# Optimization experiments

Hardware: AMD Instinct MI355X
Metric: run time of the kernel (lower is better)

## Reference

```python
import jax, jax.numpy as jnp
import numpy as np

B, T, C = 2, 2048, 2048
N_HEADS, HEAD_DIM = 16, 128
THETA = 10000.0


def _rope_cos_sin(T, dim, theta=THETA):
    inv_freq = 1.0 / (theta ** (jnp.arange(0, dim, 2, dtype=jnp.float32) / dim))  # (dim/2,)
    t = jnp.arange(T, dtype=jnp.float32)
    freqs = jnp.outer(t, inv_freq)  # (T, dim/2)
    return jnp.cos(freqs), jnp.sin(freqs)


def _apply_rope(x, cos, sin):
    # x: (B, H, T, D); cos/sin: (T, D/2) -> broadcast over B, H
    xr = x[..., 0::2]
    xi = x[..., 1::2]
    or_ = xr * cos - xi * sin
    oi_ = xr * sin + xi * cos
    return jnp.stack([or_, oi_], axis=-1).reshape(x.shape)


def setup_inputs() -> dict:
    key = jax.random.key(0)
    ks = jax.random.split(key, 5)
    scale = 1.0 / np.sqrt(C)
    x = jax.random.normal(ks[0], (B, T, C), dtype=jnp.float32)
    wq = jax.random.normal(ks[1], (C, N_HEADS * HEAD_DIM), dtype=jnp.float32) * scale
    wk = jax.random.normal(ks[2], (C, N_HEADS * HEAD_DIM), dtype=jnp.float32) * scale
    wv = jax.random.normal(ks[3], (C, N_HEADS * HEAD_DIM), dtype=jnp.float32) * scale
    wo = jax.random.normal(ks[4], (N_HEADS * HEAD_DIM, C), dtype=jnp.float32) * scale
    mask = jnp.tril(jnp.ones((T, T), dtype=bool))[None, None]  # causal (1,1,T,T)
    return {"x": x, "mask": mask, "wq": wq, "wk": wk, "wv": wv, "wo": wo}


def reference(x, mask, wq, wk, wv, wo):
    Bx, Tx, Cx = x.shape
    cos, sin = _rope_cos_sin(Tx, HEAD_DIM)
    # projections -> (B, H, T, D)
    def proj(w):
        return (x @ w).reshape(Bx, Tx, N_HEADS, HEAD_DIM).transpose(0, 2, 1, 3)
    q = _apply_rope(proj(wq), cos, sin)
    k = _apply_rope(proj(wk), cos, sin)
    v = proj(wv)
    scores = jnp.einsum("bhqd,bhkd->bhqk", q, k) / jnp.sqrt(jnp.float32(HEAD_DIM))
    scores = jnp.where(mask, scores, -jnp.inf)
    attn = jax.nn.softmax(scores, axis=-1)
    out = jnp.einsum("bhqk,bhkd->bhqd", attn, v)
    out = out.transpose(0, 2, 1, 3).reshape(Bx, Tx, Cx)
    return out @ wo
```

## Files before the change

### kernel.cpp

```cpp
#include <hip/hip_runtime.h>
#include <stdint.h>

#define B_  2
#define T_  2048
#define C_  2048
#define NH  16
#define HD  128
#define M_  (B_*T_)

typedef unsigned short ushort_t;
typedef unsigned int uint;
typedef __attribute__((ext_vector_type(8))) short short8;
typedef __attribute__((ext_vector_type(4))) float f32x4;
typedef __attribute__((ext_vector_type(16))) float f32x16;

#if __has_builtin(__builtin_amdgcn_exp2f)
#define EXP2 __builtin_amdgcn_exp2f
#else
#define EXP2 exp2f
#endif

__device__ inline ushort_t f2b(float f) {
  union { float f; unsigned u; } x; x.f = f;
  unsigned r = (x.u + 0x7fffu + ((x.u >> 16) & 1u)) >> 16;
  return (ushort_t)r;
}
__device__ inline float b2f(ushort_t b) {
  union { unsigned u; float f; } x; x.u = ((unsigned)b) << 16;
  return x.f;
}
__device__ inline uint cvtpk(float lo, float hi) {
  uint d;
  asm("v_cvt_pk_bf16_f32 %0, %1, %2" : "=v"(d) : "v"(lo), "v"(hi));
  return d;
}
__device__ inline void pl32swap(uint& a, uint& b) {
  asm volatile("v_permlane32_swap_b32 %0, %1" : "+v"(a), "+v"(b));
}
__device__ inline void gload_lds16(const void* g, void* l) {
  __builtin_amdgcn_global_load_lds((const __attribute__((address_space(1))) void*)g,
                                   (__attribute__((address_space(3))) void*)l, 16, 0, 0);
}

__global__ __launch_bounds__(256) void cvt_f32_bf16(const float* __restrict__ in,
                                                    ushort_t* __restrict__ out, int n4) {
  int i = blockIdx.x * 256 + threadIdx.x;
  if (i >= n4) return;
  float4 v = ((const float4*)in)[i];
  unsigned long long pk = (unsigned long long)f2b(v.x)
                        | ((unsigned long long)f2b(v.y) << 16)
                        | ((unsigned long long)f2b(v.z) << 32)
                        | ((unsigned long long)f2b(v.w) << 48);
  ((unsigned long long*)out)[i] = pk;
}

template<int FROM_F32>
__global__ __launch_bounds__(256) void transpose_to_bf16(const void* __restrict__ inv,
                                                         ushort_t* __restrict__ out,
                                                         int rows, int cols) {
  __shared__ __align__(16) ushort_t tile[64][72];
  const int t = threadIdx.x;
  const int br = blockIdx.y * 64, bc = blockIdx.x * 64;
  if (FROM_F32) {
    const float* in = (const float*)inv;
    const int vc = t & 15, r0 = t >> 4;
#pragma unroll
    for (int i = 0; i < 4; i++) {
      int row = r0 + 16 * i;
      float4 v = *(const float4*)&in[(size_t)(br + row) * cols + bc + vc * 4];
      tile[row][vc * 4 + 0] = f2b(v.x);
      tile[row][vc * 4 + 1] = f2b(v.y);
      tile[row][vc * 4 + 2] = f2b(v.z);
      tile[row][vc * 4 + 3] = f2b(v.w);
    }
  } else {
    const ushort_t* in = (const ushort_t*)inv;
    const int vc = t & 7, r0 = t >> 3;
#pragma unroll
    for (int i = 0; i < 2; i++) {
      int row = r0 + 32 * i;
      short8 v = *(const short8*)&in[(size_t)(br + row) * cols + bc + vc * 8];
#pragma unroll
      for (int j = 0; j < 8; j++) tile[row][vc * 8 + j] = (ushort_t)v[j];
    }
  }
  __syncthreads();
  const int oc = t >> 2;
#pragma unroll
  for (int s2 = 0; s2 < 2; s2++) {
    int seg = (t & 3) + 4 * s2;
    short8 w;
#pragma unroll
    for (int j = 0; j < 8; j++) w[j] = (short)tile[seg * 8 + j][oc];
    *(short8*)&out[(size_t)(bc + oc) * rows + br + seg * 8] = w;
  }
}

__global__ __launch_bounds__(256) void rope_table(float* __restrict__ cs, float* __restrict__ sn) {
  int i = blockIdx.x * 256 + threadIdx.x;
  int tt = i >> 6, f = i & 63;
  float inv = powf(10000.0f, -(float)(2 * f) / 128.0f);
  float ang = (float)tt * inv;
  cs[i] = cosf(ang);
  sn[i] = sinf(ang);
}

__global__ __launch_bounds__(256) void rope_apply(ushort_t* __restrict__ Q, ushort_t* __restrict__ K,
                                                  const float* __restrict__ cs,
                                                  const float* __restrict__ sn) {
  int i = blockIdx.x * 256 + threadIdx.x;
  int row = i >> 8, g = i & 255;
  int tt = row & (T_ - 1);
  int fb = (g * 4) & 63;
  f32x4 cv = *(const f32x4*)&cs[(tt << 6) + fb];
  f32x4 sv = *(const f32x4*)&sn[(tt << 6) + fb];
  size_t idx = ((size_t)row << 11) + (size_t)g * 8;
  short8 q = *(const short8*)&Q[idx];
  short8 k = *(const short8*)&K[idx];
#pragma unroll
  for (int j = 0; j < 4; j++) {
    float c = cv[j], s = sv[j];
    float qr = b2f((ushort_t)q[2 * j]), qi = b2f((ushort_t)q[2 * j + 1]);
    q[2 * j]     = (short)f2b(qr * c - qi * s);
    q[2 * j + 1] = (short)f2b(qr * s + qi * c);
    float kr = b2f((ushort_t)k[2 * j]), ki = b2f((ushort_t)k[2 * j + 1]);
    k[2 * j]     = (short)f2b(kr * c - ki * s);
    k[2 * j + 1] = (short)f2b(kr * s + ki * c);
  }
  *(short8*)&Q[idx] = q;
  *(short8*)&K[idx] = k;
}

template<int OUTF32>
__global__ __launch_bounds__(256) void gemm_bt(const ushort_t* __restrict__ A,
                                               const ushort_t* __restrict__ Bt0,
                                               const ushort_t* __restrict__ Bt1,
                                               const ushort_t* __restrict__ Bt2,
                                               void* __restrict__ O0, void* __restrict__ O1,
                                               void* __restrict__ O2, int N, int K) {
  const int z = blockIdx.z;
  const ushort_t* Bt = (z == 0) ? Bt0 : (z == 1) ? Bt1 : Bt2;
  void* Ov = (z == 0) ? O0 : (z == 1) ? O1 : O2;
  const int t = threadIdx.x;
  const int lane = t & 63, wave = t >> 6;
  const int wr = wave >> 1, wc = wave & 1;
  const int lr = lane & 15, lg = lane >> 4;
  const int bm = blockIdx.y, bn = blockIdx.x;
  __shared__ __align__(16) ushort_t As[128 * 64];
  __shared__ __align__(16) ushort_t Bs[128 * 64];
  f32x4 acc[4][4] = {};
  const ushort_t* Ap = A + (size_t)bm * 128 * K;
  const ushort_t* Bp = Bt + (size_t)bn * 128 * K;
  for (int k0 = 0; k0 < K; k0 += 64) {
#pragma unroll
    for (int i = 0; i < 4; i++) {
      int chunk = i * 256 + t;
      int row = chunk >> 3, kc = chunk & 7;
      gload_lds16(Ap + (size_t)row * K + k0 + kc * 8, &As[(size_t)(i * 256 + wave * 64) * 8]);
      gload_lds16(Bp + (size_t)row * K + k0 + kc * 8, &Bs[(size_t)(i * 256 + wave * 64) * 8]);
    }
    __syncthreads();
#pragma unroll
    for (int kk = 0; kk < 64; kk += 32) {
      short8 af[4], bf[4];
#pragma unroll
      for (int i = 0; i < 4; i++) {
        af[i] = *(const short8*)&As[(wr * 64 + i * 16 + lr) * 64 + kk + lg * 8];
        bf[i] = *(const short8*)&Bs[(wc * 64 + i * 16 + lr) * 64 + kk + lg * 8];
      }
#pragma unroll
      for (int i = 0; i < 4; i++)
#pragma unroll
        for (int j = 0; j < 4; j++)
          acc[i][j] = __builtin_amdgcn_mfma_f32_16x16x32_bf16(af[i], bf[j], acc[i][j], 0, 0, 0);
    }
    __syncthreads();
  }
  const int row0 = bm * 128 + wr * 64 + lg * 4;
  const int col0 = bn * 128 + wc * 64 + lr;
  if (OUTF32) {
    float* O = (float*)Ov;
#pragma unroll
    for (int i = 0; i < 4; i++)
#pragma unroll
      for (int j = 0; j < 4; j++)
#pragma unroll
        for (int r = 0; r < 4; r++)
          O[(size_t)(row0 + i * 16 + r) * N + col0 + j * 16] = acc[i][j][r];
  } else {
    ushort_t* O = (ushort_t*)Ov;
#pragma unroll
    for (int i = 0; i < 4; i++)
#pragma unroll
      for (int j = 0; j < 4; j++)
#pragma unroll
        for (int r = 0; r < 4; r++)
          O[(size_t)(row0 + i * 16 + r) * N + col0 + j * 16] = f2b(acc[i][j][r]);
  }
}

__global__ __launch_bounds__(64) void flash_attn3(const ushort_t* __restrict__ Q,
                                                  const ushort_t* __restrict__ K,
                                                  const ushort_t* __restrict__ Vt,
                                                  ushort_t* __restrict__ AO) {
  int flat = blockIdx.x;
  int swz = (flat & 7) * 128 + (flat >> 3);
  const int bh = swz >> 5, widx = swz & 31;
  const int b = bh >> 4, h = bh & 15;
  const int lane = threadIdx.x & 63;
  const int col = lane & 31, hi = lane >> 5, hioff = 4 * hi;
  const ushort_t* Qb = Q + (size_t)b * T_ * C_ + (size_t)h * HD;
  const ushort_t* Kb = K + (size_t)b * T_ * C_ + (size_t)h * HD;
  const ushort_t* Vb = Vt + (size_t)bh * (size_t)HD * T_;
  const float sc = 0.12754245f;

#pragma unroll 1
  for (int ph = 0; ph < 2; ph++) {
    const int tile = ph ? (63 - widx) : widx;
    const int q0 = tile * 32;
    const int qcol = q0 + col;
    short8 qf[8];
#pragma unroll
    for (int db = 0; db < 8; db++)
      qf[db] = *(const short8*)&Qb[(size_t)qcol * C_ + db * 16 + hi * 8];

    f32x16 o0 = {}, o1 = {}, o2 = {}, o3 = {};
    float m = -1e30f, l = 0.f;

    short8 kf[8];
#pragma unroll
    for (int db = 0; db < 8; db++)
      kf[db] = *(const short8*)&Kb[(size_t)col * C_ + db * 16 + hi * 8];

#pragma unroll 1
    for (int k0 = 0; k0 <= q0; k0 += 32) {
      f32x16 s = {};
#pragma unroll
      for (int db = 0; db < 8; db++)
        s = __builtin_amdgcn_mfma_f32_32x32x16_bf16(kf[db], qf[db], s, 0, 0, 0);
      if (k0 + 32 <= q0) {
#pragma unroll
        for (int db = 0; db < 8; db++)
          kf[db] = *(const short8*)&Kb[(size_t)(k0 + 32 + col) * C_ + db * 16 + hi * 8];
      }
      short8 va[4][2];
#pragma unroll
      for (int dblk = 0; dblk < 4; dblk++)
#pragma unroll
        for (int j = 0; j < 2; j++)
          va[dblk][j] = *(const short8*)&Vb[(size_t)(dblk * 32 + col) * T_ + k0 + j * 16 + hi * 8];

      const bool domask = (k0 + 31 > q0);
      if (domask) {
#pragma unroll
        for (int r = 0; r < 16; r++) {
          int krow = k0 + ((r & 3) + 8 * (r >> 2)) + hioff;
          float v = s[r] * sc;
          s[r] = (krow > qcol) ? -1e30f : v;
        }
      } else {
#pragma unroll
        for (int r = 0; r < 16; r++) s[r] = s[r] * sc;
      }
      float tm = s[0];
#pragma unroll
      for (int r = 1; r < 16; r++) tm = fmaxf(tm, s[r]);
      tm = fmaxf(tm, __shfl_xor(tm, 32, 64));
      if (!__all(tm <= m + 8.0f)) {
        float mn = fmaxf(m, tm);
        float corr = EXP2(m - mn);
        m = mn;
        l *= corr;
#pragma unroll
        for (int r = 0; r < 16; r++) { o0[r] *= corr; o1[r] *= corr; o2[r] *= corr; o3[r] *= corr; }
      }
#pragma unroll
      for (int r = 0; r < 16; r++) s[r] = EXP2(s[r] - m);
      float rs = s[0];
#pragma unroll
      for (int r = 1; r < 16; r++) rs += s[r];
      rs += __shfl_xor(rs, 32, 64);
      l += rs;
      uint c0 = cvtpk(s[0], s[1]),  c1 = cvtpk(s[2], s[3]);
      uint c2 = cvtpk(s[4], s[5]),  c3 = cvtpk(s[6], s[7]);
      uint c4 = cvtpk(s[8], s[9]),  c5 = cvtpk(s[10], s[11]);
      uint c6 = cvtpk(s[12], s[13]), c7 = cvtpk(s[14], s[15]);
      pl32swap(c0, c2); pl32swap(c1, c3);
      pl32swap(c4, c6); pl32swap(c5, c7);
      union { uint u[4]; short8 v; } pb0, pb1;
      pb0.u[0] = c0; pb0.u[1] = c1; pb0.u[2] = c2; pb0.u[3] = c3;
      pb1.u[0] = c4; pb1.u[1] = c5; pb1.u[2] = c6; pb1.u[3] = c7;
      o0 = __builtin_amdgcn_mfma_f32_32x32x16_bf16(va[0][0], pb0.v, o0, 0, 0, 0);
      o1 = __builtin_amdgcn_mfma_f32_32x32x16_bf16(va[1][0], pb0.v, o1, 0, 0, 0);
      o2 = __builtin_amdgcn_mfma_f32_32x32x16_bf16(va[2][0], pb0.v, o2, 0, 0, 0);
      o3 = __builtin_amdgcn_mfma_f32_32x32x16_bf16(va[3][0], pb0.v, o3, 0, 0, 0);
      o0 = __builtin_amdgcn_mfma_f32_32x32x16_bf16(va[0][1], pb1.v, o0, 0, 0, 0);
      o1 = __builtin_amdgcn_mfma_f32_32x32x16_bf16(va[1][1], pb1.v, o1, 0, 0, 0);
      o2 = __builtin_amdgcn_mfma_f32_32x32x16_bf16(va[2][1], pb1.v, o2, 0, 0, 0);
      o3 = __builtin_amdgcn_mfma_f32_32x32x16_bf16(va[3][1], pb1.v, o3, 0, 0, 0);
    }
    float inv = 1.0f / l;
    size_t rowbase = (size_t)(b * T_ + qcol) * C_ + h * HD;
#pragma unroll
    for (int r = 0; r < 16; r++) {
      int d = (r & 3) + 8 * (r >> 2) + hioff;
      AO[rowbase + d]      = f2b(o0[r] * inv);
      AO[rowbase + 32 + d] = f2b(o1[r] * inv);
      AO[rowbase + 64 + d] = f2b(o2[r] * inv);
      AO[rowbase + 96 + d] = f2b(o3[r] * inv);
    }
  }
}

extern "C" void kernel_launch(void* const* d_in, const int* in_sizes, int n_in,
                              void* d_out, int out_size, void* d_ws, size_t ws_size,
                              hipStream_t stream) {
  const float* x  = (const float*)d_in[0];
  const float* wq = (const float*)d_in[2];
  const float* wk = (const float*)d_in[3];
  const float* wv = (const float*)d_in[4];
  const float* wo = (const float*)d_in[5];

  char* ws = (char*)d_ws;
  size_t off = 0;
  auto alloc = [&](size_t bytes) { char* p = ws + off; off += (bytes + 255) & ~255ull; return p; };
  ushort_t* Qb  = (ushort_t*)alloc((size_t)M_ * C_ * 2);
  ushort_t* Kb  = (ushort_t*)alloc((size_t)M_ * C_ * 2);
  ushort_t* Vb  = (ushort_t*)alloc((size_t)M_ * C_ * 2);
  ushort_t* Vtb = (ushort_t*)alloc((size_t)M_ * C_ * 2);
  ushort_t* xb  = (ushort_t*)alloc((size_t)M_ * C_ * 2);
  ushort_t* AO  = xb;
  ushort_t* wqt = (ushort_t*)alloc((size_t)C_ * C_ * 2);
  ushort_t* wkt = (ushort_t*)alloc((size_t)C_ * C_ * 2);
  ushort_t* wvt = (ushort_t*)alloc((size_t)C_ * C_ * 2);
  ushort_t* wot = (ushort_t*)alloc((size_t)C_ * C_ * 2);
  float* cs = (float*)alloc((size_t)T_ * 64 * 4);
  float* sn = (float*)alloc((size_t)T_ * 64 * 4);

  cvt_f32_bf16<<<(M_ * C_ / 4 + 255) / 256, 256, 0, stream>>>(x, xb, M_ * C_ / 4);
  dim3 tg(C_ / 64, C_ / 64);
  transpose_to_bf16<1><<<tg, 256, 0, stream>>>(wq, wqt, C_, C_);
  transpose_to_bf16<1><<<tg, 256, 0, stream>>>(wk, wkt, C_, C_);
  transpose_to_bf16<1><<<tg, 256, 0, stream>>>(wv, wvt, C_, C_);
  transpose_to_bf16<1><<<tg, 256, 0, stream>>>(wo, wot, C_, C_);
  rope_table<<<T_ * 64 / 256, 256, 0, stream>>>(cs, sn);
  gemm_bt<0><<<dim3(C_ / 128, M_ / 128, 3), 256, 0, stream>>>(xb, wqt, wkt, wvt,
                                                              Qb, Kb, Vb, C_, C_);
  rope_apply<<<M_ * C_ / 8 / 256, 256, 0, stream>>>(Qb, Kb, cs, sn);
  for (int b = 0; b < B_; b++)
    transpose_to_bf16<0><<<dim3(T_ / 64, T_ / 64), 256, 0, stream>>>(
        Vb + (size_t)b * T_ * C_, Vtb + (size_t)b * T_ * C_, T_, C_);
  flash_attn3<<<dim3(B_ * NH * 32), 64, 0, stream>>>(Qb, Kb, Vtb, AO);
  gemm_bt<1><<<dim3(C_ / 128, M_ / 128, 1), 256, 0, stream>>>(AO, wot, wot, wot,
                                                              d_out, d_out, d_out, C_, C_);
  (void)in_sizes; (void)n_in; (void)out_size; (void)ws_size;
}
```

Before: 486.3 us.

## Replace GEMM with 256x256-tile double-buffered, swizzled LDS kernel

Replaces the 128x128-tile, 256-thread GEMM used for the QKV and output projections with a 256x256-tile, 512-thread kernel. The new kernel double-buffers A and B tiles in 128 KB of dynamic LDS, prefetching the next K-slice while the current one is computed. It XOR-swizzles the LDS layout to avoid bank conflicts and raises wave priority around the MFMA block. The larger tiles improve data reuse, but they cut the grid to 384 and 128 blocks. That risks leaving CUs idle, especially for the output projection, and the large LDS use limits occupancy to one block per CU.

```diff
diff --git a/kernel.cpp b/kernel.cpp
--- a/kernel.cpp
+++ b/kernel.cpp
@@ -132,70 +132,100 @@
 }
 
 template<int OUTF32>
-__global__ __launch_bounds__(256) void gemm_bt(const ushort_t* __restrict__ A,
-                                               const ushort_t* __restrict__ Bt0,
-                                               const ushort_t* __restrict__ Bt1,
-                                               const ushort_t* __restrict__ Bt2,
-                                               void* __restrict__ O0, void* __restrict__ O1,
-                                               void* __restrict__ O2, int N, int K) {
+__global__ __launch_bounds__(512, 2) void gemm_bt256(const ushort_t* __restrict__ A,
+                                                     const ushort_t* __restrict__ Bt0,
+                                                     const ushort_t* __restrict__ Bt1,
+                                                     const ushort_t* __restrict__ Bt2,
+                                                     void* __restrict__ O0, void* __restrict__ O1,
+                                                     void* __restrict__ O2, int N, int K) {
+  extern __shared__ __align__(16) ushort_t lds[];
   const int z = blockIdx.z;
   const ushort_t* Bt = (z == 0) ? Bt0 : (z == 1) ? Bt1 : Bt2;
   void* Ov = (z == 0) ? O0 : (z == 1) ? O1 : O2;
-  const int t = threadIdx.x;
-  const int lane = t & 63, wave = t >> 6;
-  const int wr = wave >> 1, wc = wave & 1;
+  const int tid = threadIdx.x;
+  const int lane = tid & 63, wave = tid >> 6;
   const int lr = lane & 15, lg = lane >> 4;
+  const int wm = wave >> 2, wn = wave & 3;
+  const int swz = lr & 7;
   const int bm = blockIdx.y, bn = blockIdx.x;
-  __shared__ __align__(16) ushort_t As[128 * 64];
-  __shared__ __align__(16) ushort_t Bs[128 * 64];
-  f32x4 acc[4][4] = {};
-  const ushort_t* Ap = A + (size_t)bm * 128 * K;
-  const ushort_t* Bp = Bt + (size_t)bn * 128 * K;
-  for (int k0 = 0; k0 < K; k0 += 64) {
+  const ushort_t* Ap = A + (size_t)bm * 256 * K;
+  const ushort_t* Bp = Bt + (size_t)bn * 256 * K;
+  const int NT = K >> 6;
+
+  f32x4 acc[8][4] = {};
+
+  auto stage8 = [&](int k0, int base) {
 #pragma unroll
     for (int i = 0; i < 4; i++) {
-      int chunk = i * 256 + t;
-      int row = chunk >> 3, kc = chunk & 7;
-      gload_lds16(Ap + (size_t)row * K + k0 + kc * 8, &As[(size_t)(i * 256 + wave * 64) * 8]);
-      gload_lds16(Bp + (size_t)row * K + k0 + kc * 8, &Bs[(size_t)(i * 256 + wave * 64) * 8]);
-    }
-    __syncthreads();
-#pragma unroll
-    for (int kk = 0; kk < 64; kk += 32) {
-      short8 af[4], bf[4];
-#pragma unroll
-      for (int i = 0; i < 4; i++) {
-        af[i] = *(const short8*)&As[(wr * 64 + i * 16 + lr) * 64 + kk + lg * 8];
-        bf[i] = *(const short8*)&Bs[(wc * 64 + i * 16 + lr) * 64 + kk + lg * 8];
-      }
-#pragma unroll
-      for (int i = 0; i < 4; i++)
-#pragma unroll
-        for (int j = 0; j < 4; j++)
-          acc[i][j] = __builtin_amdgcn_mfma_f32_16x16x32_bf16(af[i], bf[j], acc[i][j], 0, 0, 0);
-    }
-    __syncthreads();
-  }
-  const int row0 = bm * 128 + wr * 64 + lg * 4;
-  const int col0 = bn * 128 + wc * 64 + lr;
+      int idx = i * 512 + wave * 64 + lane;
+      int row = idx >> 3;
+      int c = (idx & 7) ^ (row & 7);
+      gload_lds16(Ap + (size_t)row * K + k0 + c * 8,
+                  &lds[(size_t)base + (size_t)(i * 512 + wave * 64) * 8]);
+    }
+#pragma unroll
+    for (int i = 0; i < 4; i++) {
+      int idx = i * 512 + wave * 64 + lane;
+      int row = idx >> 3;
+      int c = (idx & 7) ^ (row & 7);
+      gload_lds16(Bp + (size_t)row * K + k0 + c * 8,
+                  &lds[(size_t)base + 16384 + (size_t)(i * 512 + wave * 64) * 8]);
+    }
+  };
+
+  stage8(0, 0);
+
+  for (int t = 0; t < NT; t++) {
+    __builtin_amdgcn_s_barrier();
+    if (t + 1 < NT) {
+      stage8((t + 1) << 6, ((t + 1) & 1) * 32768);
+      asm volatile("s_waitcnt vmcnt(8)" ::: "memory");
+    } else {
+      asm volatile("s_waitcnt vmcnt(0)" ::: "memory");
+    }
+    __builtin_amdgcn_s_barrier();
+    const int abase = (t & 1) * 32768, bbase = abase + 16384;
+    __builtin_amdgcn_s_setprio(1);
+#pragma unroll
+    for (int kk = 0; kk < 2; kk++) {
+      short8 af[8], bf[4];
+#pragma unroll
+      for (int mf = 0; mf < 8; mf++)
+        af[mf] = *(const short8*)&lds[abase + (wm * 128 + mf * 16 + lr) * 64 +
+                                      (((kk * 4) + lg) ^ swz) * 8];
+#pragma unroll
+      for (int nf = 0; nf < 4; nf++)
+        bf[nf] = *(const short8*)&lds[bbase + (wn * 64 + nf * 16 + lr) * 64 +
+                                      (((kk * 4) + lg) ^ swz) * 8];
+#pragma unroll
+      for (int mf = 0; mf < 8; mf++)
+#pragma unroll
+        for (int nf = 0; nf < 4; nf++)
+          acc[mf][nf] = __builtin_amdgcn_mfma_f32_16x16x32_bf16(af[mf], bf[nf], acc[mf][nf], 0, 0, 0);
+    }
+    __builtin_amdgcn_s_setprio(0);
+  }
+
+  const int row0 = bm * 256 + wm * 128 + lg * 4;
+  const int col0 = bn * 256 + wn * 64 + lr;
   if (OUTF32) {
     float* O = (float*)Ov;
 #pragma unroll
-    for (int i = 0; i < 4; i++)
-#pragma unroll
-      for (int j = 0; j < 4; j++)
+    for (int mf = 0; mf < 8; mf++)
+#pragma unroll
+      for (int nf = 0; nf < 4; nf++)
 #pragma unroll
         for (int r = 0; r < 4; r++)
-          O[(size_t)(row0 + i * 16 + r) * N + col0 + j * 16] = acc[i][j][r];
+          O[(size_t)(row0 + mf * 16 + r) * N + col0 + nf * 16] = acc[mf][nf][r];
   } else {
     ushort_t* O = (ushort_t*)Ov;
 #pragma unroll
-    for (int i = 0; i < 4; i++)
-#pragma unroll
-      for (int j = 0; j < 4; j++)
+    for (int mf = 0; mf < 8; mf++)
+#pragma unroll
+      for (int nf = 0; nf < 4; nf++)
 #pragma unroll
         for (int r = 0; r < 4; r++)
-          O[(size_t)(row0 + i * 16 + r) * N + col0 + j * 16] = f2b(acc[i][j][r]);
+          O[(size_t)(row0 + mf * 16 + r) * N + col0 + nf * 16] = f2b(acc[mf][nf][r]);
   }
 }
 
@@ -344,14 +374,14 @@
   transpose_to_bf16<1><<<tg, 256, 0, stream>>>(wv, wvt, C_, C_);
   transpose_to_bf16<1><<<tg, 256, 0, stream>>>(wo, wot, C_, C_);
   rope_table<<<T_ * 64 / 256, 256, 0, stream>>>(cs, sn);
-  gemm_bt<0><<<dim3(C_ / 128, M_ / 128, 3), 256, 0, stream>>>(xb, wqt, wkt, wvt,
-                                                              Qb, Kb, Vb, C_, C_);
+  gemm_bt256<0><<<dim3(C_ / 256, M_ / 256, 3), 512, 131072, stream>>>(
+      xb, wqt, wkt, wvt, Qb, Kb, Vb, C_, C_);
   rope_apply<<<M_ * C_ / 8 / 256, 256, 0, stream>>>(Qb, Kb, cs, sn);
   for (int b = 0; b < B_; b++)
     transpose_to_bf16<0><<<dim3(T_ / 64, T_ / 64), 256, 0, stream>>>(
         Vb + (size_t)b * T_ * C_, Vtb + (size_t)b * T_ * C_, T_, C_);
   flash_attn3<<<dim3(B_ * NH * 32), 64, 0, stream>>>(Qb, Kb, Vtb, AO);
-  gemm_bt<1><<<dim3(C_ / 128, M_ / 128, 1), 256, 0, stream>>>(AO, wot, wot, wot,
-                                                              d_out, d_out, d_out, C_, C_);
+  gemm_bt256<1><<<dim3(C_ / 256, M_ / 256, 1), 512, 131072, stream>>>(
+      AO, wot, wot, wot, d_out, d_out, d_out, C_, C_);
   (void)in_sizes; (void)n_in; (void)out_size; (void)ws_size;
 }
```

Result: no change. 481.4 us (-1.0%).
